# Kernel optimization log

Measured on AMD Instinct MI355X. Metric: run time of the kernel, lower is better.

The kernel has to match this reference:

```python
import jax, jax.numpy as jnp
import numpy as np

IDIM = 256
N_UNITS = 512
N_LAYERS = 4
E_UNITS = 2048
H = 8
D_K = N_UNITS // H
EPS = 1e-5


def _layer_norm(x, g, b):
    mu = jnp.mean(x, axis=-1, keepdims=True)
    var = jnp.mean(jnp.square(x - mu), axis=-1, keepdims=True)
    return (x - mu) * jax.lax.rsqrt(var + EPS) * g + b


def setup_inputs() -> dict:
    key = jax.random.key(0)
    ks = jax.random.split(key, 16)
    s = 0.02
    inp = {
        'x': jax.random.normal(ks[0], (4, 2, 1024, IDIM), dtype=jnp.float32),
        'Win': jax.random.normal(ks[1], (N_UNITS, IDIM), dtype=jnp.float32) * s,
        'bin_': jnp.zeros((N_UNITS,), jnp.float32),
        'ln1_g': jnp.ones((N_LAYERS, N_UNITS), jnp.float32),
        'ln1_b': jnp.zeros((N_LAYERS, N_UNITS), jnp.float32),
        'Wq': jax.random.normal(ks[2], (N_LAYERS, N_UNITS, N_UNITS), dtype=jnp.float32) * s,
        'bq': jnp.zeros((N_LAYERS, N_UNITS), jnp.float32),
        'Wk': jax.random.normal(ks[3], (N_LAYERS, N_UNITS, N_UNITS), dtype=jnp.float32) * s,
        'bk': jnp.zeros((N_LAYERS, N_UNITS), jnp.float32),
        'Wv': jax.random.normal(ks[4], (N_LAYERS, N_UNITS, N_UNITS), dtype=jnp.float32) * s,
        'bv': jnp.zeros((N_LAYERS, N_UNITS), jnp.float32),
        'Wo': jax.random.normal(ks[5], (N_LAYERS, N_UNITS, N_UNITS), dtype=jnp.float32) * s,
        'bo': jnp.zeros((N_LAYERS, N_UNITS), jnp.float32),
        'ln2_g': jnp.ones((N_LAYERS, N_UNITS), jnp.float32),
        'ln2_b': jnp.zeros((N_LAYERS, N_UNITS), jnp.float32),
        'W1': jax.random.normal(ks[6], (N_LAYERS, E_UNITS, N_UNITS), dtype=jnp.float32) * s,
        'b1': jnp.zeros((N_LAYERS, E_UNITS), jnp.float32),
        'W2': jax.random.normal(ks[7], (N_LAYERS, N_UNITS, E_UNITS), dtype=jnp.float32) * s,
        'b2': jnp.zeros((N_LAYERS, N_UNITS), jnp.float32),
        'lno_g': jnp.ones((N_UNITS,), jnp.float32),
        'lno_b': jnp.zeros((N_UNITS,), jnp.float32),
    }
    return inp


def reference(x, Win, bin_, ln1_g, ln1_b, Wq, bq, Wk, bk, Wv, bv, Wo, bo,
              ln2_g, ln2_b, W1, b1, W2, b2, lno_g, lno_b):
    bs, num, T, dim = x.shape
    B = bs * num
    # input projection; e is kept as [B*T, n_units] like the torch code
    e = x.reshape(B * T, dim) @ Win.T + bin_
    scale = 1.0 / np.sqrt(D_K).astype(np.float32)
    for i in range(N_LAYERS):
        e = _layer_norm(e, ln1_g[i], ln1_b[i])
        # multi-head self-attention (dropout is identity in eval)
        q = (e @ Wq[i].T + bq[i]).reshape(B, T, H, D_K)
        k = (e @ Wk[i].T + bk[i]).reshape(B, T, H, D_K)
        v = (e @ Wv[i].T + bv[i]).reshape(B, T, H, D_K)
        scores = jnp.einsum('bthd,bshd->bhts', q, k) * scale  # [B,H,T,T]
        att = jax.nn.softmax(scores, axis=-1)
        ctx = jnp.einsum('bhts,bshd->bthd', att, v).reshape(B * T, N_UNITS)
        s = ctx @ Wo[i].T + bo[i]
        e = e + s
        e = _layer_norm(e, ln2_g[i], ln2_b[i])
        # position-wise feed-forward
        hdn = jnp.maximum(e @ W1[i].T + b1[i], 0.0)
        e = e + (hdn @ W2[i].T + b2[i])
    out = _layer_norm(e, lno_g, lno_b)
    return out.reshape(bs, num, T, N_UNITS)
```

## Files before the change

kernel.cpp:

```cpp
#include <hip/hip_runtime.h>
#include <hip/hip_bf16.h>
#include <math.h>
#include <stdint.h>

#define IDIM   256
#define NU     512
#define NL     4
#define EU     2048
#define NH     8
#define DK     64
#define TT     1024
#define NB     8
#define MTOT   8192

typedef short  bf16x8 __attribute__((ext_vector_type(8)));
typedef float  f32x4  __attribute__((ext_vector_type(4)));
typedef unsigned short ushortv2 __attribute__((ext_vector_type(2)));

__device__ __forceinline__ unsigned short f2b(float x) {
  unsigned int u = __float_as_uint(x);
  u += 0x7fffu + ((u >> 16) & 1u);
  return (unsigned short)(u >> 16);
}

__device__ __forceinline__ void gload16(const unsigned short* g, unsigned short* l) {
  auto gp = reinterpret_cast<const __attribute__((address_space(1))) unsigned int*>(
      reinterpret_cast<uintptr_t>(g));
  auto lp = reinterpret_cast<__attribute__((address_space(3))) unsigned int*>(
      reinterpret_cast<uintptr_t>(l));
  __builtin_amdgcn_global_load_lds(gp, lp, 16, 0, 0);
}

__global__ __launch_bounds__(256) void cvt_bf16(
    const float* __restrict__ src, unsigned short* __restrict__ dst, int n) {
  int i = (blockIdx.x * 256 + threadIdx.x) * 8;
  if (i >= n) return;
  float4 a = *(const float4*)(src + i);
  float4 b = *(const float4*)(src + i + 4);
  bf16x8 r;
  r[0] = (short)f2b(a.x); r[1] = (short)f2b(a.y);
  r[2] = (short)f2b(a.z); r[3] = (short)f2b(a.w);
  r[4] = (short)f2b(b.x); r[5] = (short)f2b(b.y);
  r[6] = (short)f2b(b.z); r[7] = (short)f2b(b.w);
  *(bf16x8*)(dst + i) = r;
}

#define GEMM_STAGE(BUF, KK)                                                  \
  _Pragma("unroll") for (int ii = 0; ii < 2; ++ii) {                         \
    gload16(ag + (size_t)(ii * 64) * kdim + (KK), &As[BUF][ii * 2048 + wv * 512]); \
    gload16(bg + (size_t)(ii * 64) * kdim + (KK), &Bs[BUF][ii * 2048 + wv * 512]); \
  }

#define GEMM_CORE(K_, KBEG, KEND)                                            \
  __shared__ unsigned short As[2][128 * 32];                                 \
  __shared__ unsigned short Bs[2][128 * 32];                                 \
  const int kdim = (K_);                                                     \
  const int tid  = threadIdx.x;                                              \
  const int lane = tid & 63;                                                 \
  const int wv   = tid >> 6;                                                 \
  const int wm   = (wv >> 1) * 64;                                           \
  const int wn   = (wv & 1) * 64;                                            \
  const int fr   = lane & 15;                                                \
  const int fc   = lane >> 4;                                                \
  const int srow = wv * 16 + (lane >> 2);                                    \
  const int skk  = (lane & 3) * 8;                                           \
  const unsigned short* ag = A + (size_t)(m0 + srow) * kdim + skk;           \
  const unsigned short* bg = W + (size_t)(n0 + srow) * kdim + skk;           \
  f32x4 acc[4][4];                                                           \
  _Pragma("unroll") for (int i = 0; i < 4; ++i)                              \
    _Pragma("unroll") for (int j = 0; j < 4; ++j)                            \
      acc[i][j] = (f32x4){0.f, 0.f, 0.f, 0.f};                               \
  int cur = 0;                                                               \
  GEMM_STAGE(0, (KBEG))                                                      \
  for (int k0 = (KBEG); k0 < (KEND); k0 += 32) {                             \
    __syncthreads();   \
    if (k0 + 32 < (KEND)) { GEMM_STAGE(cur ^ 1, k0 + 32) }                   \
    const unsigned short* acu = As[cur];                                     \
    const unsigned short* bcu = Bs[cur];                                     \
    bf16x8 af[4], bfr[4];                                                    \
    _Pragma("unroll") for (int mi = 0; mi < 4; ++mi)                         \
      af[mi] = *(const bf16x8*)&acu[(wm + mi * 16 + fr) * 32 + fc * 8];      \
    _Pragma("unroll") for (int ni = 0; ni < 4; ++ni)                         \
      bfr[ni] = *(const bf16x8*)&bcu[(wn + ni * 16 + fr) * 32 + fc * 8];     \
    _Pragma("unroll") for (int mi = 0; mi < 4; ++mi)                         \
      _Pragma("unroll") for (int ni = 0; ni < 4; ++ni)                       \
        acc[mi][ni] = __builtin_amdgcn_mfma_f32_16x16x32_bf16(               \
            af[mi], bfr[ni], acc[mi][ni], 0, 0, 0);                          \
    cur ^= 1;                                                                \
  }

template<int MODE, bool RELU>
__global__ __launch_bounds__(256) void gemm_bf(
    const unsigned short* __restrict__ A, const unsigned short* __restrict__ W,
    const float* __restrict__ bias, float* __restrict__ Cf,
    unsigned short* __restrict__ Cb, int M, int N, int K, int kchunk) {
  const int m0 = blockIdx.y * 128;
  const int n0 = blockIdx.x * 128;
  const int kbeg = blockIdx.z * kchunk;
  const int kend = kbeg + kchunk;
  GEMM_CORE(K, kbeg, kend)

  const bool addb = (blockIdx.z == 0);
#pragma unroll
  for (int ni = 0; ni < 4; ++ni) {
    const int col = n0 + wn + ni * 16 + fr;
    const float bb = (MODE != 2 || addb) ? bias[col] : 0.f;
#pragma unroll
    for (int mi = 0; mi < 4; ++mi) {
      const int row = m0 + wm + mi * 16 + fc * 4;
#pragma unroll
      for (int j = 0; j < 4; ++j) {
        size_t off = (size_t)(row + j) * N + col;
        float r = acc[mi][ni][j] + bb;
        if (RELU) r = fmaxf(r, 0.f);
        if (MODE == 0) Cf[off] = r;
        else if (MODE == 1) Cb[off] = f2b(r);
        else atomicAdd(&Cf[off], r);
      }
    }
  }
}

__global__ __launch_bounds__(256) void gemm_qkv(
    const unsigned short* __restrict__ A,
    const unsigned short* __restrict__ Wq, const unsigned short* __restrict__ Wk,
    const unsigned short* __restrict__ Wv,
    const float* __restrict__ bq, const float* __restrict__ bk,
    const float* __restrict__ bv,
    unsigned short* __restrict__ Oq, unsigned short* __restrict__ Ok,
    unsigned short* __restrict__ Ov) {
  const int zz = blockIdx.z;
  const unsigned short* W  = zz == 0 ? Wq : (zz == 1 ? Wk : Wv);
  const float* bias        = zz == 0 ? bq : (zz == 1 ? bk : bv);
  unsigned short* C        = zz == 0 ? Oq : (zz == 1 ? Ok : Ov);
  const float scale        = zz == 0 ? 0.125f : 1.0f;
  const int m0 = blockIdx.y * 128;
  const int n0 = blockIdx.x * 128;
  GEMM_CORE(NU, 0, NU)

#pragma unroll
  for (int ni = 0; ni < 4; ++ni) {
    const int col = n0 + wn + ni * 16 + fr;
    const float bb = bias[col];
#pragma unroll
    for (int mi = 0; mi < 4; ++mi) {
      const int row = m0 + wm + mi * 16 + fc * 4;
#pragma unroll
      for (int j = 0; j < 4; ++j)
        C[(size_t)(row + j) * NU + col] = f2b((acc[mi][ni][j] + bb) * scale);
    }
  }
}

template<bool WB>
__global__ __launch_bounds__(256) void layernorm_inplace(
    float* __restrict__ e, const float* __restrict__ g,
    const float* __restrict__ b, unsigned short* __restrict__ eb) {
  const int row = blockIdx.x;
  float* x = e + (size_t)row * NU;
  const int tid = threadIdx.x;

  float2 v = *(const float2*)&x[tid * 2];
  float sum = v.x + v.y;
  float sq  = v.x * v.x + v.y * v.y;
#pragma unroll
  for (int o = 32; o > 0; o >>= 1) {
    sum += __shfl_down(sum, o);
    sq  += __shfl_down(sq, o);
  }
  __shared__ float ps[4], pq[4], stat[2];
  const int wid = tid >> 6, lane = tid & 63;
  if (lane == 0) { ps[wid] = sum; pq[wid] = sq; }
  __syncthreads();
  if (tid == 0) {
    float s = ps[0] + ps[1] + ps[2] + ps[3];
    float q = pq[0] + pq[1] + pq[2] + pq[3];
    float mu = s * (1.0f / NU);
    float var = q * (1.0f / NU) - mu * mu;
    stat[0] = mu;
    stat[1] = rsqrtf(var + 1e-5f);
  }
  __syncthreads();
  const float mu = stat[0], rstd = stat[1];
  const float2 gg = *(const float2*)&g[tid * 2];
  const float2 bb = *(const float2*)&b[tid * 2];
  v.x = (v.x - mu) * rstd * gg.x + bb.x;
  v.y = (v.y - mu) * rstd * gg.y + bb.y;
  *(float2*)&x[tid * 2] = v;
  if (WB) {
    ushortv2 o = {f2b(v.x), f2b(v.y)};
    *(ushortv2*)&eb[(size_t)row * NU + tid * 2] = o;
  }
}

__global__ __launch_bounds__(256) void flash_attn_mfma(
    const unsigned short* __restrict__ Q, const unsigned short* __restrict__ K,
    const unsigned short* __restrict__ V, unsigned short* __restrict__ O) {
  constexpr int LSTR = 72;
  constexpr int VSTR = 66;
  __shared__ unsigned short Ks[64 * LSTR];
  __shared__ unsigned short Vt[64 * VSTR];
  __shared__ unsigned short Ps[64 * LSTR];

  const int b = blockIdx.z, h = blockIdx.y;
  const int q0 = blockIdx.x * 64;
  const int tid = threadIdx.x;
  const int lane = tid & 63;
  const int w = tid >> 6;
  const int fr = lane & 15;
  const int fc = lane >> 4;

  const size_t hb = ((size_t)b * TT) * NU + h * DK;

  bf16x8 qf[2];
#pragma unroll
  for (int kc = 0; kc < 2; ++kc)
    qf[kc] = *(const bf16x8*)(Q + hb +
        (size_t)(q0 + w * 16 + fr) * NU + kc * 32 + fc * 8);

  f32x4 ctx[4];
#pragma unroll
  for (int ni = 0; ni < 4; ++ni) ctx[ni] = (f32x4){0.f, 0.f, 0.f, 0.f};
  float m_run[4], l_run[4];
#pragma unroll
  for (int j = 0; j < 4; ++j) { m_run[j] = -1e30f; l_run[j] = 0.f; }

  const int sr = tid >> 2;
  const int sd = (tid & 3) * 16;

  for (int kt = 0; kt < TT; kt += 64) {
    const unsigned short* kp = K + hb + (size_t)(kt + sr) * NU + sd;
    const unsigned short* vp = V + hb + (size_t)(kt + sr) * NU + sd;
    bf16x8 k0 = *(const bf16x8*)kp, k1 = *(const bf16x8*)(kp + 8);
    bf16x8 v0 = *(const bf16x8*)vp, v1 = *(const bf16x8*)(vp + 8);

    __syncthreads();
    *(bf16x8*)&Ks[sr * LSTR + sd]     = k0;
    *(bf16x8*)&Ks[sr * LSTR + sd + 8] = k1;
#pragma unroll
    for (int t = 0; t < 8; ++t) {
      Vt[(sd + t)     * VSTR + sr] = (unsigned short)v0[t];
      Vt[(sd + t + 8) * VSTR + sr] = (unsigned short)v1[t];
    }
    __syncthreads();

    bf16x8 kf[4][2];
#pragma unroll
    for (int ni = 0; ni < 4; ++ni)
#pragma unroll
      for (int kc = 0; kc < 2; ++kc)
        kf[ni][kc] = *(const bf16x8*)&Ks[(ni * 16 + fr) * LSTR + kc * 32 + fc * 8];

    f32x4 sacc[4];
#pragma unroll
    for (int ni = 0; ni < 4; ++ni) sacc[ni] = (f32x4){0.f, 0.f, 0.f, 0.f};
#pragma unroll
    for (int kc = 0; kc < 2; ++kc)
#pragma unroll
      for (int ni = 0; ni < 4; ++ni)
        sacc[ni] = __builtin_amdgcn_mfma_f32_16x16x32_bf16(
            qf[kc], kf[ni][kc], sacc[ni], 0, 0, 0);

    float cm[4];
#pragma unroll
    for (int j = 0; j < 4; ++j)
      cm[j] = fmaxf(fmaxf(sacc[0][j], sacc[1][j]),
                    fmaxf(sacc[2][j], sacc[3][j]));
#pragma unroll
    for (int mask = 1; mask < 16; mask <<= 1)
#pragma unroll
      for (int j = 0; j < 4; ++j)
        cm[j] = fmaxf(cm[j], __shfl_xor(cm[j], mask));

    int need = (cm[0] > m_run[0] + 8.f) | (cm[1] > m_run[1] + 8.f) |
               (cm[2] > m_run[2] + 8.f) | (cm[3] > m_run[3] + 8.f);
    if (__any(need)) {
#pragma unroll
      for (int j = 0; j < 4; ++j) {
        float mn = fmaxf(m_run[j], cm[j]);
        float corr = __expf(m_run[j] - mn);
        m_run[j] = mn;
        l_run[j] *= corr;
#pragma unroll
        for (int ni = 0; ni < 4; ++ni) ctx[ni][j] *= corr;
      }
    }
#pragma unroll
    for (int j = 0; j < 4; ++j)
#pragma unroll
      for (int ni = 0; ni < 4; ++ni) {
        float p = __expf(sacc[ni][j] - m_run[j]);
        l_run[j] += p;
        Ps[(w * 16 + fc * 4 + j) * LSTR + ni * 16 + fr] = f2b(p);
      }

    bf16x8 pf[2], vf[4][2];
#pragma unroll
    for (int kc = 0; kc < 2; ++kc)
      pf[kc] = *(const bf16x8*)&Ps[(w * 16 + fr) * LSTR + kc * 32 + fc * 8];
#pragma unroll
    for (int ni = 0; ni < 4; ++ni)
#pragma unroll
      for (int kc = 0; kc < 2; ++kc)
        vf[ni][kc] = *(const bf16x8*)&Vt[(ni * 16 + fr) * VSTR + kc * 32 + fc * 8];
#pragma unroll
    for (int kc = 0; kc < 2; ++kc)
#pragma unroll
      for (int ni = 0; ni < 4; ++ni)
        ctx[ni] = __builtin_amdgcn_mfma_f32_16x16x32_bf16(
            pf[kc], vf[ni][kc], ctx[ni], 0, 0, 0);
  }

#pragma unroll
  for (int j = 0; j < 4; ++j) {
    float l = l_run[j];
#pragma unroll
    for (int mask = 1; mask < 16; mask <<= 1)
      l += __shfl_xor(l, mask);
    const float inv = 1.0f / l;
    const int row = q0 + w * 16 + fc * 4 + j;
    unsigned short* dst = O + hb + (size_t)row * NU;
#pragma unroll
    for (int ni = 0; ni < 4; ++ni)
      dst[ni * 16 + fr] = f2b(ctx[ni][j] * inv);
  }
}

extern "C" void kernel_launch(void* const* d_in, const int* in_sizes, int n_in,
                              void* d_out, int out_size, void* d_ws, size_t ws_size,
                              hipStream_t stream) {
  const float* x     = (const float*)d_in[0];
  const float* Win   = (const float*)d_in[1];
  const float* bin_  = (const float*)d_in[2];
  const float* ln1_g = (const float*)d_in[3];
  const float* ln1_b = (const float*)d_in[4];
  const float* Wq    = (const float*)d_in[5];
  const float* bq    = (const float*)d_in[6];
  const float* Wk    = (const float*)d_in[7];
  const float* bk    = (const float*)d_in[8];
  const float* Wv    = (const float*)d_in[9];
  const float* bv    = (const float*)d_in[10];
  const float* Wo    = (const float*)d_in[11];
  const float* bo    = (const float*)d_in[12];
  const float* ln2_g = (const float*)d_in[13];
  const float* ln2_b = (const float*)d_in[14];
  const float* W1    = (const float*)d_in[15];
  const float* b1    = (const float*)d_in[16];
  const float* W2    = (const float*)d_in[17];
  const float* b2    = (const float*)d_in[18];
  const float* lno_g = (const float*)d_in[19];
  const float* lno_b = (const float*)d_in[20];

  float* e = (float*)d_out;
  unsigned short* wsb = (unsigned short*)d_ws;
  const size_t M1 = 1u << 20;
  unsigned short* q    = wsb;
  unsigned short* k    = wsb + 4 * M1;
  unsigned short* v    = wsb + 8 * M1;
  unsigned short* ctx  = wsb + 12 * M1;
  unsigned short* hdn  = wsb;
  unsigned short* xbf  = wsb + 4 * M1;
  unsigned short* winb = wsb + 6 * M1;
  unsigned short* ebf  = wsb + 16 * M1;
  unsigned short* wqb  = wsb + 20 * M1;
  unsigned short* wkb  = wsb + 21 * M1;
  unsigned short* wvb  = wsb + 22 * M1;
  unsigned short* wob  = wsb + 23 * M1;
  unsigned short* w1b  = wsb + 24 * M1;
  unsigned short* w2b  = wsb + 28 * M1;

  const dim3 blk(256);
  cvt_bf16<<<1024, blk, 0, stream>>>(x,   xbf,  MTOT * IDIM);
  cvt_bf16<<<64,   blk, 0, stream>>>(Win, winb, NU * IDIM);
  cvt_bf16<<<512,  blk, 0, stream>>>(Wq,  wqb,  NL * NU * NU);
  cvt_bf16<<<512,  blk, 0, stream>>>(Wk,  wkb,  NL * NU * NU);
  cvt_bf16<<<512,  blk, 0, stream>>>(Wv,  wvb,  NL * NU * NU);
  cvt_bf16<<<512,  blk, 0, stream>>>(Wo,  wob,  NL * NU * NU);
  cvt_bf16<<<2048, blk, 0, stream>>>(W1,  w1b,  NL * EU * NU);
  cvt_bf16<<<2048, blk, 0, stream>>>(W2,  w2b,  NL * NU * EU);

  const dim3 gProjIn(NU / 128, MTOT / 128);
  const dim3 gQKV(NU / 128, MTOT / 128, 3);
  const dim3 gWo(NU / 128, MTOT / 128, 4);
  const dim3 gF1(EU / 128, MTOT / 128);
  const dim3 gF2(NU / 128, MTOT / 128, 4);
  const dim3 gAttn(TT / 64, NH, NB);

  gemm_bf<0, false><<<gProjIn, blk, 0, stream>>>(
      xbf, winb, bin_, e, nullptr, MTOT, NU, IDIM, IDIM);

  for (int i = 0; i < NL; ++i) {
    layernorm_inplace<true><<<MTOT, blk, 0, stream>>>(e, ln1_g + i * NU, ln1_b + i * NU, ebf);

    gemm_qkv<<<gQKV, blk, 0, stream>>>(ebf, wqb + (size_t)i * NU * NU,
                                       wkb + (size_t)i * NU * NU,
                                       wvb + (size_t)i * NU * NU,
                                       bq + i * NU, bk + i * NU, bv + i * NU,
                                       q, k, v);

    flash_attn_mfma<<<gAttn, blk, 0, stream>>>(q, k, v, ctx);

    gemm_bf<2, false><<<gWo, blk, 0, stream>>>(
        ctx, wob + (size_t)i * NU * NU, bo + i * NU, e, nullptr,
        MTOT, NU, NU, NU / 4);

    layernorm_inplace<true><<<MTOT, blk, 0, stream>>>(e, ln2_g + i * NU, ln2_b + i * NU, ebf);

    gemm_bf<1, true><<<gF1, blk, 0, stream>>>(
        ebf, w1b + (size_t)i * EU * NU, b1 + i * EU, nullptr, hdn,
        MTOT, EU, NU, NU);

    gemm_bf<2, false><<<gF2, blk, 0, stream>>>(
        hdn, w2b + (size_t)i * NU * EU, b2 + i * NU, e, nullptr,
        MTOT, NU, EU, EU / 4);
  }

  layernorm_inplace<false><<<MTOT, blk, 0, stream>>>(e, lno_g, lno_b, nullptr);
}
```

Measured before the change: 1.212 ms.

## Replace LDS-direct double buffering with register-prefetch padded LDS, add 128x64 GEMM tiles

The GEMM core drops the global_load_lds double-buffered staging. Each K step now prefetches the next tile into registers and stores it into a single padded LDS buffer (row stride 40) to avoid bank conflicts, with two barriers per step. A new 128x64-tile variant is used for the N=512 GEMMs (input projection, QKV, Wo, FFN2), and the split-K factor for Wo and FFN2 drops from 4 to 2, which means fewer atomic adds into the output. In exchange there is an extra barrier per iteration, higher register use for the prefetch, and less reuse of each loaded tile in the narrower variant.

```diff
diff --git a/kernel.cpp b/kernel.cpp
--- a/kernel.cpp
+++ b/kernel.cpp
@@ -21,14 +21,6 @@
   unsigned int u = __float_as_uint(x);
   u += 0x7fffu + ((u >> 16) & 1u);
   return (unsigned short)(u >> 16);
-}
-
-__device__ __forceinline__ void gload16(const unsigned short* g, unsigned short* l) {
-  auto gp = reinterpret_cast<const __attribute__((address_space(1))) unsigned int*>(
-      reinterpret_cast<uintptr_t>(g));
-  auto lp = reinterpret_cast<__attribute__((address_space(3))) unsigned int*>(
-      reinterpret_cast<uintptr_t>(l));
-  __builtin_amdgcn_global_load_lds(gp, lp, 16, 0, 0);
 }
 
 __global__ __launch_bounds__(256) void cvt_bf16(
@@ -45,15 +37,10 @@
   *(bf16x8*)(dst + i) = r;
 }
 
-#define GEMM_STAGE(BUF, KK)                                                  \
-  _Pragma("unroll") for (int ii = 0; ii < 2; ++ii) {                         \
-    gload16(ag + (size_t)(ii * 64) * kdim + (KK), &As[BUF][ii * 2048 + wv * 512]); \
-    gload16(bg + (size_t)(ii * 64) * kdim + (KK), &Bs[BUF][ii * 2048 + wv * 512]); \
-  }
-
 #define GEMM_CORE(K_, KBEG, KEND)                                            \
-  __shared__ unsigned short As[2][128 * 32];                                 \
-  __shared__ unsigned short Bs[2][128 * 32];                                 \
+  constexpr int LSTR = 40;                                                   \
+  __shared__ unsigned short As[128 * LSTR];                                  \
+  __shared__ unsigned short Bs[128 * LSTR];                                  \
   const int kdim = (K_);                                                     \
   const int tid  = threadIdx.x;                                              \
   const int lane = tid & 63;                                                 \
@@ -62,31 +49,90 @@
   const int wn   = (wv & 1) * 64;                                            \
   const int fr   = lane & 15;                                                \
   const int fc   = lane >> 4;                                                \
-  const int srow = wv * 16 + (lane >> 2);                                    \
-  const int skk  = (lane & 3) * 8;                                           \
-  const unsigned short* ag = A + (size_t)(m0 + srow) * kdim + skk;           \
-  const unsigned short* bg = W + (size_t)(n0 + srow) * kdim + skk;           \
+  const int sr   = tid >> 1;                                                 \
+  const int sh   = (tid & 1) * 16;                                           \
+  const short* aptr = (const short*)A + (size_t)(m0 + sr) * kdim + sh;       \
+  const short* wptr = (const short*)W + (size_t)(n0 + sr) * kdim + sh;       \
+  short* asd = (short*)&As[sr * LSTR + sh];                                  \
+  short* bsd = (short*)&Bs[sr * LSTR + sh];                                  \
   f32x4 acc[4][4];                                                           \
   _Pragma("unroll") for (int i = 0; i < 4; ++i)                              \
     _Pragma("unroll") for (int j = 0; j < 4; ++j)                            \
       acc[i][j] = (f32x4){0.f, 0.f, 0.f, 0.f};                               \
-  int cur = 0;                                                               \
-  GEMM_STAGE(0, (KBEG))                                                      \
+  bf16x8 pa0 = *(const bf16x8*)(aptr + (KBEG));                              \
+  bf16x8 pa1 = *(const bf16x8*)(aptr + (KBEG) + 8);                          \
+  bf16x8 pb0 = *(const bf16x8*)(wptr + (KBEG));                              \
+  bf16x8 pb1 = *(const bf16x8*)(wptr + (KBEG) + 8);                          \
   for (int k0 = (KBEG); k0 < (KEND); k0 += 32) {                             \
-    __syncthreads();   \
-    if (k0 + 32 < (KEND)) { GEMM_STAGE(cur ^ 1, k0 + 32) }                   \
-    const unsigned short* acu = As[cur];                                     \
-    const unsigned short* bcu = Bs[cur];                                     \
+    __syncthreads();                                                         \
+    *(bf16x8*)asd = pa0;  *(bf16x8*)(asd + 8) = pa1;                         \
+    *(bf16x8*)bsd = pb0;  *(bf16x8*)(bsd + 8) = pb1;                         \
+    __syncthreads();                                                         \
+    const int kn = k0 + 32;                                                  \
+    if (kn < (KEND)) {                                                       \
+      pa0 = *(const bf16x8*)(aptr + kn);                                     \
+      pa1 = *(const bf16x8*)(aptr + kn + 8);                                 \
+      pb0 = *(const bf16x8*)(wptr + kn);                                     \
+      pb1 = *(const bf16x8*)(wptr + kn + 8);                                 \
+    }                                                                        \
     bf16x8 af[4], bfr[4];                                                    \
     _Pragma("unroll") for (int mi = 0; mi < 4; ++mi)                         \
-      af[mi] = *(const bf16x8*)&acu[(wm + mi * 16 + fr) * 32 + fc * 8];      \
+      af[mi] = *(const bf16x8*)&As[(wm + mi * 16 + fr) * LSTR + fc * 8];     \
     _Pragma("unroll") for (int ni = 0; ni < 4; ++ni)                         \
-      bfr[ni] = *(const bf16x8*)&bcu[(wn + ni * 16 + fr) * 32 + fc * 8];     \
+      bfr[ni] = *(const bf16x8*)&Bs[(wn + ni * 16 + fr) * LSTR + fc * 8];    \
     _Pragma("unroll") for (int mi = 0; mi < 4; ++mi)                         \
       _Pragma("unroll") for (int ni = 0; ni < 4; ++ni)                       \
         acc[mi][ni] = __builtin_amdgcn_mfma_f32_16x16x32_bf16(               \
             af[mi], bfr[ni], acc[mi][ni], 0, 0, 0);                          \
-    cur ^= 1;                                                                \
+  }
+
+#define GEMM_CORE64(K_, KBEG, KEND)                                          \
+  constexpr int LSTR = 40;                                                   \
+  __shared__ unsigned short As[128 * LSTR];                                  \
+  __shared__ unsigned short Bs[64 * LSTR];                                   \
+  const int kdim = (K_);                                                     \
+  const int tid  = threadIdx.x;                                              \
+  const int lane = tid & 63;                                                 \
+  const int wv   = tid >> 6;                                                 \
+  const int wm   = (wv >> 1) * 64;                                           \
+  const int wn   = (wv & 1) * 32;                                            \
+  const int fr   = lane & 15;                                                \
+  const int fc   = lane >> 4;                                                \
+  const int sr   = tid >> 1;                                                 \
+  const int sh   = (tid & 1) * 16;                                           \
+  const int sr2  = tid >> 2;                                                 \
+  const int sh2  = (tid & 3) * 8;                                            \
+  const short* aptr = (const short*)A + (size_t)(m0 + sr) * kdim + sh;       \
+  const short* wptr = (const short*)W + (size_t)(n0 + sr2) * kdim + sh2;     \
+  short* asd = (short*)&As[sr * LSTR + sh];                                  \
+  short* bsd = (short*)&Bs[sr2 * LSTR + sh2];                                \
+  f32x4 acc[4][2];                                                           \
+  _Pragma("unroll") for (int i = 0; i < 4; ++i)                              \
+    _Pragma("unroll") for (int j = 0; j < 2; ++j)                            \
+      acc[i][j] = (f32x4){0.f, 0.f, 0.f, 0.f};                               \
+  bf16x8 pa0 = *(const bf16x8*)(aptr + (KBEG));                              \
+  bf16x8 pa1 = *(const bf16x8*)(aptr + (KBEG) + 8);                          \
+  bf16x8 pb0 = *(const bf16x8*)(wptr + (KBEG));                              \
+  for (int k0 = (KBEG); k0 < (KEND); k0 += 32) {                             \
+    __syncthreads();                                                         \
+    *(bf16x8*)asd = pa0;  *(bf16x8*)(asd + 8) = pa1;                         \
+    *(bf16x8*)bsd = pb0;                                                     \
+    __syncthreads();                                                         \
+    const int kn = k0 + 32;                                                  \
+    if (kn < (KEND)) {                                                       \
+      pa0 = *(const bf16x8*)(aptr + kn);                                     \
+      pa1 = *(const bf16x8*)(aptr + kn + 8);                                 \
+      pb0 = *(const bf16x8*)(wptr + kn);                                     \
+    }                                                                        \
+    bf16x8 af[4], bfr[2];                                                    \
+    _Pragma("unroll") for (int mi = 0; mi < 4; ++mi)                         \
+      af[mi] = *(const bf16x8*)&As[(wm + mi * 16 + fr) * LSTR + fc * 8];     \
+    _Pragma("unroll") for (int ni = 0; ni < 2; ++ni)                         \
+      bfr[ni] = *(const bf16x8*)&Bs[(wn + ni * 16 + fr) * LSTR + fc * 8];    \
+    _Pragma("unroll") for (int mi = 0; mi < 4; ++mi)                         \
+      _Pragma("unroll") for (int ni = 0; ni < 2; ++ni)                       \
+        acc[mi][ni] = __builtin_amdgcn_mfma_f32_16x16x32_bf16(               \
+            af[mi], bfr[ni], acc[mi][ni], 0, 0, 0);                          \
   }
 
 template<int MODE, bool RELU>
@@ -121,7 +167,39 @@
   }
 }
 
-__global__ __launch_bounds__(256) void gemm_qkv(
+template<int MODE, bool RELU>
+__global__ __launch_bounds__(256) void gemm_bf64(
+    const unsigned short* __restrict__ A, const unsigned short* __restrict__ W,
+    const float* __restrict__ bias, float* __restrict__ Cf,
+    unsigned short* __restrict__ Cb, int M, int N, int K, int kchunk) {
+  const int m0 = blockIdx.y * 128;
+  const int n0 = blockIdx.x * 64;
+  const int kbeg = blockIdx.z * kchunk;
+  const int kend = kbeg + kchunk;
+  GEMM_CORE64(K, kbeg, kend)
+
+  const bool addb = (blockIdx.z == 0);
+#pragma unroll
+  for (int ni = 0; ni < 2; ++ni) {
+    const int col = n0 + wn + ni * 16 + fr;
+    const float bb = (MODE != 2 || addb) ? bias[col] : 0.f;
+#pragma unroll
+    for (int mi = 0; mi < 4; ++mi) {
+      const int row = m0 + wm + mi * 16 + fc * 4;
+#pragma unroll
+      for (int j = 0; j < 4; ++j) {
+        size_t off = (size_t)(row + j) * N + col;
+        float r = acc[mi][ni][j] + bb;
+        if (RELU) r = fmaxf(r, 0.f);
+        if (MODE == 0) Cf[off] = r;
+        else if (MODE == 1) Cb[off] = f2b(r);
+        else atomicAdd(&Cf[off], r);
+      }
+    }
+  }
+}
+
+__global__ __launch_bounds__(256) void gemm_qkv64(
     const unsigned short* __restrict__ A,
     const unsigned short* __restrict__ Wq, const unsigned short* __restrict__ Wk,
     const unsigned short* __restrict__ Wv,
@@ -135,11 +213,11 @@
   unsigned short* C        = zz == 0 ? Oq : (zz == 1 ? Ok : Ov);
   const float scale        = zz == 0 ? 0.125f : 1.0f;
   const int m0 = blockIdx.y * 128;
-  const int n0 = blockIdx.x * 128;
-  GEMM_CORE(NU, 0, NU)
-
-#pragma unroll
-  for (int ni = 0; ni < 4; ++ni) {
+  const int n0 = blockIdx.x * 64;
+  GEMM_CORE64(NU, 0, NU)
+
+#pragma unroll
+  for (int ni = 0; ni < 2; ++ni) {
     const int col = n0 + wn + ni * 16 + fr;
     const float bb = bias[col];
 #pragma unroll
@@ -379,30 +457,30 @@
   cvt_bf16<<<2048, blk, 0, stream>>>(W1,  w1b,  NL * EU * NU);
   cvt_bf16<<<2048, blk, 0, stream>>>(W2,  w2b,  NL * NU * EU);
 
-  const dim3 gProjIn(NU / 128, MTOT / 128);
-  const dim3 gQKV(NU / 128, MTOT / 128, 3);
-  const dim3 gWo(NU / 128, MTOT / 128, 4);
+  const dim3 gProjIn(NU / 64, MTOT / 128);
+  const dim3 gQKV(NU / 64, MTOT / 128, 3);
+  const dim3 gWo(NU / 64, MTOT / 128, 2);
   const dim3 gF1(EU / 128, MTOT / 128);
-  const dim3 gF2(NU / 128, MTOT / 128, 4);
+  const dim3 gF2(NU / 64, MTOT / 128, 2);
   const dim3 gAttn(TT / 64, NH, NB);
 
-  gemm_bf<0, false><<<gProjIn, blk, 0, stream>>>(
+  gemm_bf64<0, false><<<gProjIn, blk, 0, stream>>>(
       xbf, winb, bin_, e, nullptr, MTOT, NU, IDIM, IDIM);
 
   for (int i = 0; i < NL; ++i) {
     layernorm_inplace<true><<<MTOT, blk, 0, stream>>>(e, ln1_g + i * NU, ln1_b + i * NU, ebf);
 
-    gemm_qkv<<<gQKV, blk, 0, stream>>>(ebf, wqb + (size_t)i * NU * NU,
-                                       wkb + (size_t)i * NU * NU,
-                                       wvb + (size_t)i * NU * NU,
-                                       bq + i * NU, bk + i * NU, bv + i * NU,
-                                       q, k, v);
+    gemm_qkv64<<<gQKV, blk, 0, stream>>>(ebf, wqb + (size_t)i * NU * NU,
+                                         wkb + (size_t)i * NU * NU,
+                                         wvb + (size_t)i * NU * NU,
+                                         bq + i * NU, bk + i * NU, bv + i * NU,
+                                         q, k, v);
 
     flash_attn_mfma<<<gAttn, blk, 0, stream>>>(q, k, v, ctx);
 
-    gemm_bf<2, false><<<gWo, blk, 0, stream>>>(
+    gemm_bf64<2, false><<<gWo, blk, 0, stream>>>(
         ctx, wob + (size_t)i * NU * NU, bo + i * NU, e, nullptr,
-        MTOT, NU, NU, NU / 4);
+        MTOT, NU, NU, NU / 2);
 
     layernorm_inplace<true><<<MTOT, blk, 0, stream>>>(e, ln2_g + i * NU, ln2_b + i * NU, ebf);
 
@@ -410,9 +488,9 @@
         ebf, w1b + (size_t)i * EU * NU, b1 + i * EU, nullptr, hdn,
         MTOT, EU, NU, NU);
 
-    gemm_bf<2, false><<<gF2, blk, 0, stream>>>(
+    gemm_bf64<2, false><<<gF2, blk, 0, stream>>>(
         hdn, w2b + (size_t)i * NU * EU, b2 + i * NU, e, nullptr,
-        MTOT, NU, EU, EU / 4);
+        MTOT, NU, EU, EU / 2);
   }
 
   layernorm_inplace<false><<<MTOT, blk, 0, stream>>>(e, lno_g, lno_b, nullptr);
```

Result: faster. 1.110 ms (-8.4%).
